# Kernel optimization log

Hardware: AMD Instinct MI355X
Metric: run time of the kernel (lower is better)

Reference implementation:

```python
import jax, jax.numpy as jnp
import numpy as np
from jax import lax

B, C_IN, H, W = 32, 3, 224, 224
EMBED = 768 // 4  # dim // 4 = 192
K = 3             # kernel_size
STRIDE = 2        # patch_stride
PAD = 1           # patch_padding
BN_EPS = 1e-5


def setup_inputs() -> dict:
    key = jax.random.key(0)
    kx, kw, kb, kg, kbeta = jax.random.split(key, 5)
    x = jax.random.normal(kx, (B, C_IN, H, W), dtype=jnp.float32)
    fan_in = C_IN * K * K
    bound = 1.0 / np.sqrt(fan_in)
    conv_w = jax.random.uniform(kw, (EMBED, C_IN, K, K), jnp.float32, -bound, bound)
    conv_b = jax.random.uniform(kb, (EMBED,), jnp.float32, -bound, bound)
    gamma = jnp.ones((EMBED,), jnp.float32)
    beta = jnp.zeros((EMBED,), jnp.float32)
    return {"x": x, "conv_w": conv_w, "conv_b": conv_b, "gamma": gamma, "beta": beta}


def _patch_embed(x, conv_w, conv_b, gamma, beta):
    # Conv2d(in_chans, embed_dim, k=3, stride=2, pad=1)
    y = lax.conv_general_dilated(
        x, conv_w,
        window_strides=(STRIDE, STRIDE),
        padding=[(PAD, PAD), (PAD, PAD)],
        dimension_numbers=("NCHW", "OIHW", "NCHW"),
    ) + conv_b[None, :, None, None]  # [B, EMBED, 112, 112]
    # BatchNorm2d (training mode: batch statistics, biased variance)
    mean = jnp.mean(y, axis=(0, 2, 3), keepdims=True)
    var = jnp.mean(jnp.square(y - mean), axis=(0, 2, 3), keepdims=True)
    y = (y - mean) * lax.rsqrt(var + BN_EPS)
    y = y * gamma[None, :, None, None] + beta[None, :, None, None]
    # GELU (torch default: exact erf form)
    y = jax.nn.gelu(y, approximate=False)
    # MaxPool2d(kernel=3, stride=2, padding=1)
    y = lax.reduce_window(
        y, -jnp.inf, lax.max,
        window_dimensions=(1, 1, 3, 3),
        window_strides=(1, 1, STRIDE, STRIDE),
        padding=[(0, 0), (0, 0), (PAD, PAD), (PAD, PAD)],
    )  # [B, EMBED, 56, 56]
    return y


def reference(x, conv_w, conv_b, gamma, beta):
    return _patch_embed(x, conv_w, conv_b, gamma, beta)
```

## Files before the change

kernel.cpp:

```cpp
#include <hip/hip_runtime.h>
#include <hip/hip_bf16.h>
#include <math.h>

#define B_   32
#define CIN  3
#define H_   224
#define W_   224
#define OC   192
#define OH   112
#define OW   112
#define PH   56
#define PW   56
#define NSP  (B_*OH*OW)
#define PLANE (OH*OW)
#define OCG  4
#define OCPG (OC / OCG)

static __device__ __forceinline__ unsigned short f2bf(float f) {
    __hip_bfloat16 h = __float2bfloat16(f);
    return *reinterpret_cast<unsigned short*>(&h);
}
static __device__ __forceinline__ float bf_lo(unsigned int u) {
    unsigned int v = u << 16;
    return *reinterpret_cast<float*>(&v);
}
static __device__ __forceinline__ float bf_hi(unsigned int u) {
    unsigned int v = u & 0xffff0000u;
    return *reinterpret_cast<float*>(&v);
}

static __device__ __forceinline__ float fexp2(float x) {
#if __has_builtin(__builtin_amdgcn_exp2f)
    return __builtin_amdgcn_exp2f(x);
#else
    return exp2f(x);
#endif
}
static __device__ __forceinline__ float frcp(float x) {
#if __has_builtin(__builtin_amdgcn_rcpf)
    return __builtin_amdgcn_rcpf(x);
#else
    return 1.0f / x;
#endif
}

static __device__ __forceinline__ float fast_gelu(float x) {
    float x2 = x * x;
    float inner = fmaf(0.044715f * x2, x, x);
    float e = fexp2(inner * 2.3022082f);
    float r = frcp(1.0f + e);
    return x * (e * r);
}

__global__ void zero_stats(float* stats) {
    for (int i = threadIdx.x; i < 384; i += 256) stats[i] = 0.f;
}

__global__ __launch_bounds__(256) void conv_kernel(
    const float* __restrict__ x, const float* __restrict__ w,
    const float* __restrict__ bias, __hip_bfloat16* __restrict__ y)
{
    int ocg = blockIdx.x / 392;
    int sg  = (blockIdx.x - ocg * 392) * 256 + threadIdx.x;
    int owg = sg % 28;
    int t   = sg / 28;
    int oh  = t % OH;
    int b   = t / OH;

    int ih0 = 2 * oh - 1;
    int s   = (owg > 0) ? (8 * owg - 4) : 0;

    float taps[CIN][3][9];
    #pragma unroll
    for (int c = 0; c < CIN; ++c) {
        #pragma unroll
        for (int r = 0; r < 3; ++r) {
            int ih = ih0 + r;
            bool rv = (ih >= 0) && (ih < H_);
            const float* base =
                x + (((size_t)b * CIN + c) * H_ + (rv ? ih : 0)) * W_;
            float4 La = *reinterpret_cast<const float4*>(base + s);
            float4 Lb = *reinterpret_cast<const float4*>(base + (8 * owg));
            float4 Lc = *reinterpret_cast<const float4*>(base + (8 * owg + 4));
            float L[12] = {La.x, La.y, La.z, La.w, Lb.x, Lb.y, Lb.z, Lb.w,
                           Lc.x, Lc.y, Lc.z, Lc.w};
            #pragma unroll
            for (int j = 0; j < 9; ++j)
                taps[c][r][j] = rv ? L[3 + j] : 0.f;
            if (owg == 0) taps[c][r][0] = 0.f;
        }
    }

    int oc0 = ocg * OCPG;
    unsigned short* yp = reinterpret_cast<unsigned short*>(y) +
                         ((size_t)b * OC + oc0) * PLANE + oh * OW + 4 * owg;

    #pragma unroll 2
    for (int l = 0; l < OCPG; ++l) {
        int oc = oc0 + l;
        float bs = bias[oc];
        float a0 = bs, a1 = bs, a2 = bs, a3 = bs;
        const float* wp = w + oc * 27;
        #pragma unroll
        for (int c = 0; c < CIN; ++c)
            #pragma unroll
            for (int r = 0; r < 3; ++r)
                #pragma unroll
                for (int k = 0; k < 3; ++k) {
                    float wv = wp[c * 9 + r * 3 + k];
                    a0 = fmaf(wv, taps[c][r][k + 0], a0);
                    a1 = fmaf(wv, taps[c][r][k + 2], a1);
                    a2 = fmaf(wv, taps[c][r][k + 4], a2);
                    a3 = fmaf(wv, taps[c][r][k + 6], a3);
                }
        ushort4 p;
        p.x = f2bf(a0); p.y = f2bf(a1); p.z = f2bf(a2); p.w = f2bf(a3);
        *reinterpret_cast<ushort4*>(yp + (size_t)l * PLANE) = p;
    }
}

__global__ __launch_bounds__(256) void stats_kernel(
    const __hip_bfloat16* __restrict__ y, float* __restrict__ stats)
{
    int plane = blockIdx.x;
    int oc = plane % OC;
    const unsigned int* p =
        reinterpret_cast<const unsigned int*>(y) + plane * (PLANE / 2);

    float s = 0.f, s2 = 0.f;
    for (int ch = threadIdx.x; ch < PLANE / 8; ch += 256) {
        uint4 v = reinterpret_cast<const uint4*>(p)[ch];
        unsigned int u[4] = {v.x, v.y, v.z, v.w};
        #pragma unroll
        for (int k = 0; k < 4; ++k) {
            float lo = bf_lo(u[k]);
            float hi = bf_hi(u[k]);
            s  += lo + hi;
            s2 += lo * lo + hi * hi;
        }
    }

    __shared__ float ls[256], ls2[256];
    int tid = threadIdx.x;
    ls[tid] = s; ls2[tid] = s2;
    __syncthreads();
    for (int off = 128; off > 0; off >>= 1) {
        if (tid < off) { ls[tid] += ls[tid + off]; ls2[tid] += ls2[tid + off]; }
        __syncthreads();
    }
    if (tid == 0) {
        atomicAdd(&stats[oc], ls[0]);
        atomicAdd(&stats[OC + oc], ls2[0]);
    }
}

__global__ __launch_bounds__(256) void pool_kernel(
    const __hip_bfloat16* __restrict__ y, const float* __restrict__ stats,
    const float* __restrict__ gamma, const float* __restrict__ beta,
    float* __restrict__ out)
{
    int g = blockIdx.x * 256 + threadIdx.x;
    int j = g % 7;
    int t = g / 7;
    int ph = t % PH;
    int plane = t / PH;
    int oc = plane % OC;

    const unsigned short* py =
        reinterpret_cast<const unsigned short*>(y) + (size_t)plane * PLANE;

    float cmin[8], cmax[8];
    #pragma unroll
    for (int m = 0; m < 8; ++m) { cmin[m] = INFINITY; cmax[m] = -INFINITY; }

    #pragma unroll
    for (int rr = 0; rr < 3; ++rr) {
        int ih = 2 * ph - 1 + rr;
        if (ih >= 0) {
            const uint4* rp = reinterpret_cast<const uint4*>(py + ih * OW + 16 * j - 8);
            uint4 u0 = rp[0], u1 = rp[1], u2 = rp[2];
            float L[24];
            L[0]=bf_lo(u0.x); L[1]=bf_hi(u0.x); L[2]=bf_lo(u0.y); L[3]=bf_hi(u0.y);
            L[4]=bf_lo(u0.z); L[5]=bf_hi(u0.z); L[6]=bf_lo(u0.w); L[7]=bf_hi(u0.w);
            L[8]=bf_lo(u1.x); L[9]=bf_hi(u1.x); L[10]=bf_lo(u1.y); L[11]=bf_hi(u1.y);
            L[12]=bf_lo(u1.z); L[13]=bf_hi(u1.z); L[14]=bf_lo(u1.w); L[15]=bf_hi(u1.w);
            L[16]=bf_lo(u2.x); L[17]=bf_hi(u2.x); L[18]=bf_lo(u2.y); L[19]=bf_hi(u2.y);
            L[20]=bf_lo(u2.z); L[21]=bf_hi(u2.z); L[22]=bf_lo(u2.w); L[23]=bf_hi(u2.w);

            float l7min = (j == 0) ? INFINITY  : L[7];
            float l7max = (j == 0) ? -INFINITY : L[7];

            cmin[0] = fminf(cmin[0], fminf(fminf(l7min, L[8]), L[9]));
            cmax[0] = fmaxf(cmax[0], fmaxf(fmaxf(l7max, L[8]), L[9]));
            #pragma unroll
            for (int m = 1; m < 8; ++m) {
                cmin[m] = fminf(cmin[m], fminf(fminf(L[7+2*m], L[8+2*m]), L[9+2*m]));
                cmax[m] = fmaxf(cmax[m], fmaxf(fmaxf(L[7+2*m], L[8+2*m]), L[9+2*m]));
            }
        }
    }

    float mean = stats[oc] * (1.0f / (float)NSP);
    float var  = fmaf(-mean, mean, stats[OC + oc] * (1.0f / (float)NSP));
    float inv  = rsqrtf(var + 1e-5f);
    float sc   = gamma[oc] * inv;
    float sh   = fmaf(-mean, sc, beta[oc]);

    float res[8];
    #pragma unroll
    for (int m = 0; m < 8; ++m) {
        float lo = fmaf(cmin[m], sc, sh);
        float hi = fmaf(cmax[m], sc, sh);
        res[m] = fmaxf(fast_gelu(lo), fast_gelu(hi));
    }

    float* ob = out + (size_t)plane * (PH * PW) + ph * PW + 8 * j;
    float4 r0 = {res[0], res[1], res[2], res[3]};
    float4 r1 = {res[4], res[5], res[6], res[7]};
    *reinterpret_cast<float4*>(ob)     = r0;
    *reinterpret_cast<float4*>(ob + 4) = r1;
}

extern "C" void kernel_launch(void* const* d_in, const int* in_sizes, int n_in,
                              void* d_out, int out_size, void* d_ws, size_t ws_size,
                              hipStream_t stream) {
    const float* x     = (const float*)d_in[0];
    const float* w     = (const float*)d_in[1];
    const float* bias  = (const float*)d_in[2];
    const float* gamma = (const float*)d_in[3];
    const float* beta  = (const float*)d_in[4];
    float* out = (float*)d_out;

    float* stats = (float*)d_ws;
    __hip_bfloat16* y = (__hip_bfloat16*)((char*)d_ws + 4096);

    hipLaunchKernelGGL(zero_stats, dim3(1), dim3(256), 0, stream, stats);
    hipLaunchKernelGGL(conv_kernel, dim3(OCG * 392), dim3(256), 0, stream,
                       x, w, bias, y);
    hipLaunchKernelGGL(stats_kernel, dim3(B_ * OC), dim3(256), 0, stream, y, stats);
    hipLaunchKernelGGL(pool_kernel, dim3(B_ * OC * PH * 7 / 256), dim3(256), 0,
                       stream, y, stats, gamma, beta, out);
}
```

Before: 234.5 us.

## Compute conv via bf16 MFMA and fuse BN statistics into conv epilogue

Recasts the 3x3 stride-2 convolution as a small GEMM (27 taps plus a bias column padded to K=32) run on 16x16x32 bf16 MFMA instructions, with inputs and weights rounded to bf16. The BN sum and sum-of-squares are reduced from the accumulators in the conv kernel with shuffles, shared memory and atomics, which removes the separate stats pass that reread y. Output tiles are staged through padded LDS so y is stored with coalesced 16-byte writes. The cost is lower-precision conv inputs and weights, and per-lane gather loads for the im2col taps.

```diff
diff --git a/kernel.cpp b/kernel.cpp
--- a/kernel.cpp
+++ b/kernel.cpp
@@ -13,8 +13,10 @@
 #define PW   56
 #define NSP  (B_*OH*OW)
 #define PLANE (OH*OW)
-#define OCG  4
-#define OCPG (OC / OCG)
+#define CB_STRIDE 68
+
+typedef __attribute__((ext_vector_type(8))) short bf16x8;
+typedef __attribute__((ext_vector_type(4))) float f32x4;
 
 static __device__ __forceinline__ unsigned short f2bf(float f) {
     __hip_bfloat16 h = __float2bfloat16(f);
@@ -52,105 +54,155 @@
     return x * (e * r);
 }
 
+template<int K>
+static __device__ __forceinline__ float tapT(const float* __restrict__ xb,
+                                             int ihb, int iwb) {
+    if constexpr (K == 27) { return 1.0f; }
+    else if constexpr (K > 27) { return 0.0f; }
+    else {
+        constexpr int c = K / 9, r = (K % 9) / 3, j = K % 3;
+        int ih = ihb + r, iw = iwb + j;
+        bool v = ((unsigned)ih < (unsigned)H_) && ((unsigned)iw < (unsigned)W_);
+        return v ? xb[(c * H_ + ih) * W_ + iw] : 0.0f;
+    }
+}
+
 __global__ void zero_stats(float* stats) {
-    for (int i = threadIdx.x; i < 384; i += 256) stats[i] = 0.f;
+    if (threadIdx.x < 384) stats[threadIdx.x] = 0.f;
 }
 
 __global__ __launch_bounds__(256) void conv_kernel(
     const float* __restrict__ x, const float* __restrict__ w,
-    const float* __restrict__ bias, __hip_bfloat16* __restrict__ y)
+    const float* __restrict__ bias, __hip_bfloat16* __restrict__ y,
+    float* __restrict__ stats)
 {
-    int ocg = blockIdx.x / 392;
-    int sg  = (blockIdx.x - ocg * 392) * 256 + threadIdx.x;
-    int owg = sg % 28;
-    int t   = sg / 28;
-    int oh  = t % OH;
-    int b   = t / OH;
-
-    int ih0 = 2 * oh - 1;
-    int s   = (owg > 0) ? (8 * owg - 4) : 0;
-
-    float taps[CIN][3][9];
-    #pragma unroll
-    for (int c = 0; c < CIN; ++c) {
+    __shared__ __align__(16) unsigned int cbuf[OC * CB_STRIDE];
+    __shared__ float ssum[2][4 * OC];
+
+    int blk  = blockIdx.x;
+    int b    = blk / 98;
+    int pb   = (blk - b * 98) * 128;
+    int tid  = threadIdx.x;
+    int wv   = tid >> 6;
+    int lane = tid & 63;
+    int lo16 = lane & 15;
+    int kg   = lane >> 4;
+
+    bf16x8 Bf[12];
+    #pragma unroll
+    for (int n = 0; n < 12; ++n) {
+        int col = n * 16 + lo16;
+        float tw[8];
+        if (kg < 3) {
+            int base = col * 27 + kg * 8;
+            #pragma unroll
+            for (int j = 0; j < 8; ++j) tw[j] = w[base + j];
+        } else {
+            tw[0] = w[col * 27 + 24];
+            tw[1] = w[col * 27 + 25];
+            tw[2] = w[col * 27 + 26];
+            tw[3] = bias[col];
+            tw[4] = 0.f; tw[5] = 0.f; tw[6] = 0.f; tw[7] = 0.f;
+        }
         #pragma unroll
-        for (int r = 0; r < 3; ++r) {
-            int ih = ih0 + r;
-            bool rv = (ih >= 0) && (ih < H_);
-            const float* base =
-                x + (((size_t)b * CIN + c) * H_ + (rv ? ih : 0)) * W_;
-            float4 La = *reinterpret_cast<const float4*>(base + s);
-            float4 Lb = *reinterpret_cast<const float4*>(base + (8 * owg));
-            float4 Lc = *reinterpret_cast<const float4*>(base + (8 * owg + 4));
-            float L[12] = {La.x, La.y, La.z, La.w, Lb.x, Lb.y, Lb.z, Lb.w,
-                           Lc.x, Lc.y, Lc.z, Lc.w};
-            #pragma unroll
-            for (int j = 0; j < 9; ++j)
-                taps[c][r][j] = rv ? L[3 + j] : 0.f;
-            if (owg == 0) taps[c][r][0] = 0.f;
-        }
-    }
-
-    int oc0 = ocg * OCPG;
-    unsigned short* yp = reinterpret_cast<unsigned short*>(y) +
-                         ((size_t)b * OC + oc0) * PLANE + oh * OW + 4 * owg;
-
-    #pragma unroll 2
-    for (int l = 0; l < OCPG; ++l) {
-        int oc = oc0 + l;
-        float bs = bias[oc];
-        float a0 = bs, a1 = bs, a2 = bs, a3 = bs;
-        const float* wp = w + oc * 27;
+        for (int j = 0; j < 8; ++j) Bf[n][j] = (short)f2bf(tw[j]);
+    }
+
+    const float* xb = x + (size_t)b * CIN * H_ * W_;
+    bf16x8 Af[2];
+    #pragma unroll
+    for (int s = 0; s < 2; ++s) {
+        int p  = pb + wv * 32 + s * 16 + lo16;
+        int oh = p / OW;
+        int ow = p - oh * OW;
+        int ihb = 2 * oh - 1, iwb = 2 * ow - 1;
+        float tv[8];
+        if (kg == 0) {
+            tv[0]=tapT<0>(xb,ihb,iwb); tv[1]=tapT<1>(xb,ihb,iwb);
+            tv[2]=tapT<2>(xb,ihb,iwb); tv[3]=tapT<3>(xb,ihb,iwb);
+            tv[4]=tapT<4>(xb,ihb,iwb); tv[5]=tapT<5>(xb,ihb,iwb);
+            tv[6]=tapT<6>(xb,ihb,iwb); tv[7]=tapT<7>(xb,ihb,iwb);
+        } else if (kg == 1) {
+            tv[0]=tapT<8>(xb,ihb,iwb);  tv[1]=tapT<9>(xb,ihb,iwb);
+            tv[2]=tapT<10>(xb,ihb,iwb); tv[3]=tapT<11>(xb,ihb,iwb);
+            tv[4]=tapT<12>(xb,ihb,iwb); tv[5]=tapT<13>(xb,ihb,iwb);
+            tv[6]=tapT<14>(xb,ihb,iwb); tv[7]=tapT<15>(xb,ihb,iwb);
+        } else if (kg == 2) {
+            tv[0]=tapT<16>(xb,ihb,iwb); tv[1]=tapT<17>(xb,ihb,iwb);
+            tv[2]=tapT<18>(xb,ihb,iwb); tv[3]=tapT<19>(xb,ihb,iwb);
+            tv[4]=tapT<20>(xb,ihb,iwb); tv[5]=tapT<21>(xb,ihb,iwb);
+            tv[6]=tapT<22>(xb,ihb,iwb); tv[7]=tapT<23>(xb,ihb,iwb);
+        } else {
+            tv[0]=tapT<24>(xb,ihb,iwb); tv[1]=tapT<25>(xb,ihb,iwb);
+            tv[2]=tapT<26>(xb,ihb,iwb); tv[3]=tapT<27>(xb,ihb,iwb);
+            tv[4]=tapT<28>(xb,ihb,iwb); tv[5]=tapT<29>(xb,ihb,iwb);
+            tv[6]=tapT<30>(xb,ihb,iwb); tv[7]=tapT<31>(xb,ihb,iwb);
+        }
         #pragma unroll
-        for (int c = 0; c < CIN; ++c)
-            #pragma unroll
-            for (int r = 0; r < 3; ++r)
-                #pragma unroll
-                for (int k = 0; k < 3; ++k) {
-                    float wv = wp[c * 9 + r * 3 + k];
-                    a0 = fmaf(wv, taps[c][r][k + 0], a0);
-                    a1 = fmaf(wv, taps[c][r][k + 2], a1);
-                    a2 = fmaf(wv, taps[c][r][k + 4], a2);
-                    a3 = fmaf(wv, taps[c][r][k + 6], a3);
-                }
-        ushort4 p;
-        p.x = f2bf(a0); p.y = f2bf(a1); p.z = f2bf(a2); p.w = f2bf(a3);
-        *reinterpret_cast<ushort4*>(yp + (size_t)l * PLANE) = p;
-    }
-}
-
-__global__ __launch_bounds__(256) void stats_kernel(
-    const __hip_bfloat16* __restrict__ y, float* __restrict__ stats)
-{
-    int plane = blockIdx.x;
-    int oc = plane % OC;
-    const unsigned int* p =
-        reinterpret_cast<const unsigned int*>(y) + plane * (PLANE / 2);
-
-    float s = 0.f, s2 = 0.f;
-    for (int ch = threadIdx.x; ch < PLANE / 8; ch += 256) {
-        uint4 v = reinterpret_cast<const uint4*>(p)[ch];
-        unsigned int u[4] = {v.x, v.y, v.z, v.w};
+        for (int j = 0; j < 8; ++j) Af[s][j] = (short)f2bf(tv[j]);
+    }
+
+    f32x4 acc0[12], acc1[12];
+    #pragma unroll
+    for (int n = 0; n < 12; ++n) {
+        acc0[n] = (f32x4){0.f, 0.f, 0.f, 0.f};
+        acc1[n] = (f32x4){0.f, 0.f, 0.f, 0.f};
+    }
+    #pragma unroll
+    for (int n = 0; n < 12; ++n) {
+        acc0[n] = __builtin_amdgcn_mfma_f32_16x16x32_bf16(Af[0], Bf[n], acc0[n], 0, 0, 0);
+        acc1[n] = __builtin_amdgcn_mfma_f32_16x16x32_bf16(Af[1], Bf[n], acc1[n], 0, 0, 0);
+    }
+
+    #pragma unroll
+    for (int n = 0; n < 12; ++n) {
+        float s = 0.f, s2 = 0.f;
         #pragma unroll
-        for (int k = 0; k < 4; ++k) {
-            float lo = bf_lo(u[k]);
-            float hi = bf_hi(u[k]);
-            s  += lo + hi;
-            s2 += lo * lo + hi * hi;
-        }
-    }
-
-    __shared__ float ls[256], ls2[256];
-    int tid = threadIdx.x;
-    ls[tid] = s; ls2[tid] = s2;
+        for (int i = 0; i < 4; ++i) {
+            float v = acc0[n][i]; s += v; s2 = fmaf(v, v, s2);
+            v = acc1[n][i];       s += v; s2 = fmaf(v, v, s2);
+        }
+        s  += __shfl_xor(s, 16);  s  += __shfl_xor(s, 32);
+        s2 += __shfl_xor(s2, 16); s2 += __shfl_xor(s2, 32);
+        if (lane < 16) {
+            ssum[0][wv * OC + n * 16 + lane] = s;
+            ssum[1][wv * OC + n * 16 + lane] = s2;
+        }
+    }
+
+    #pragma unroll
+    for (int n = 0; n < 12; ++n) {
+        int oc = n * 16 + lo16;
+        int pu = wv * 16 + kg * 2;
+        unsigned u01 = (unsigned)f2bf(acc0[n][0]) | ((unsigned)f2bf(acc0[n][1]) << 16);
+        unsigned u23 = (unsigned)f2bf(acc0[n][2]) | ((unsigned)f2bf(acc0[n][3]) << 16);
+        cbuf[oc * CB_STRIDE + pu]     = u01;
+        cbuf[oc * CB_STRIDE + pu + 1] = u23;
+        unsigned v01 = (unsigned)f2bf(acc1[n][0]) | ((unsigned)f2bf(acc1[n][1]) << 16);
+        unsigned v23 = (unsigned)f2bf(acc1[n][2]) | ((unsigned)f2bf(acc1[n][3]) << 16);
+        cbuf[oc * CB_STRIDE + pu + 8] = v01;
+        cbuf[oc * CB_STRIDE + pu + 9] = v23;
+    }
+
     __syncthreads();
-    for (int off = 128; off > 0; off >>= 1) {
-        if (tid < off) { ls[tid] += ls[tid + off]; ls2[tid] += ls2[tid + off]; }
-        __syncthreads();
-    }
-    if (tid == 0) {
-        atomicAdd(&stats[oc], ls[0]);
-        atomicAdd(&stats[OC + oc], ls2[0]);
+
+    unsigned short* yus = reinterpret_cast<unsigned short*>(y);
+    int ocr = tid >> 4;
+    int ch  = tid & 15;
+    #pragma unroll
+    for (int ocb = 0; ocb < 12; ++ocb) {
+        int oc = ocb * 16 + ocr;
+        uint4 v = *reinterpret_cast<uint4*>(&cbuf[oc * CB_STRIDE + ch * 4]);
+        *reinterpret_cast<uint4*>(
+            yus + (size_t)(b * OC + oc) * PLANE + pb + ch * 8) = v;
+    }
+
+    for (int i = tid; i < 2 * OC; i += 256) {
+        int which = (i >= OC) ? 1 : 0;
+        int oc = i - which * OC;
+        float v = ssum[which][oc] + ssum[which][OC + oc] +
+                  ssum[which][2 * OC + oc] + ssum[which][3 * OC + oc];
+        atomicAdd(&stats[which * OC + oc], v);
     }
 }
 
@@ -234,10 +286,9 @@
     float* stats = (float*)d_ws;
     __hip_bfloat16* y = (__hip_bfloat16*)((char*)d_ws + 4096);
 
-    hipLaunchKernelGGL(zero_stats, dim3(1), dim3(256), 0, stream, stats);
-    hipLaunchKernelGGL(conv_kernel, dim3(OCG * 392), dim3(256), 0, stream,
-                       x, w, bias, y);
-    hipLaunchKernelGGL(stats_kernel, dim3(B_ * OC), dim3(256), 0, stream, y, stats);
+    hipLaunchKernelGGL(zero_stats, dim3(1), dim3(384), 0, stream, stats);
+    hipLaunchKernelGGL(conv_kernel, dim3(B_ * 98), dim3(256), 0, stream,
+                       x, w, bias, y, stats);
     hipLaunchKernelGGL(pool_kernel, dim3(B_ * OC * PH * 7 / 256), dim3(256), 0,
                        stream, y, stats, gamma, beta, out);
 }
```

Result: faster. 223.6 us (-4.7%).
